# Optimization experiments

Measured on AMD Instinct MI355X. Metric: run time of the kernel, lower is better.

## Reference

```python
import jax, jax.numpy as jnp
import numpy as np

NUM_HEADS = 10
LN_EPS = 1e-5


def setup_inputs() -> dict:
    key = jax.random.key(0)
    ks = jax.random.split(key, 6)
    N, D = 4096, 640  # in_dim == out_dim required by residual add
    x = jax.random.normal(ks[0], (N, D), dtype=jnp.float32)
    s = 1.0 / np.sqrt(D)
    Wq = jax.random.normal(ks[1], (D, D), dtype=jnp.float32) * s  # torch Linear weight [out,in]
    Wk = jax.random.normal(ks[2], (D, D), dtype=jnp.float32) * s
    Wv = jax.random.normal(ks[3], (D, D), dtype=jnp.float32) * s
    gamma = jnp.ones((D,), dtype=jnp.float32)
    beta = jnp.zeros((D,), dtype=jnp.float32)
    return {"x": x, "Wq": Wq, "Wk": Wk, "Wv": Wv, "gamma": gamma, "beta": beta}


def reference(x, Wq, Wk, Wv, gamma, beta):
    N, D = x.shape
    dk = D // NUM_HEADS
    Q = x @ Wq.T  # [N, D]
    K = x @ Wk.T
    V = x @ Wv.T
    # Faithful to source: raw reshapes (NOT transposes)
    Qh = Q.reshape(NUM_HEADS, N, dk)
    Kh = K.reshape(NUM_HEADS, N, dk).reshape(NUM_HEADS, dk, N)  # torch.reshape, not .mT
    Vh = V.reshape(NUM_HEADS, N, dk)
    # Faithful quirk: scale by sqrt(K.shape[2]) == sqrt(N)
    scale = np.float32(np.sqrt(N))
    wghts = jax.nn.softmax((Qh @ Kh) / scale, axis=-1)  # [H, N, N]
    values = wghts @ Vh  # [H, N, dk]
    values = values.reshape(N, NUM_HEADS * dk)  # raw reshape merge
    values = values + x  # residual
    # LayerNorm(out_dim), biased variance, eps=1e-5
    mean = jnp.mean(values, axis=-1, keepdims=True)
    var = jnp.mean(jnp.square(values - mean), axis=-1, keepdims=True)
    out = (values - mean) * jax.lax.rsqrt(var + LN_EPS) * gamma + beta
    return out
```

## Files before the change

### kernel.cpp

```cpp
#include <hip/hip_runtime.h>


typedef __bf16 bf16x8 __attribute__((ext_vector_type(8)));
typedef __bf16 bf16x4 __attribute__((ext_vector_type(4)));
typedef float  f32x4  __attribute__((ext_vector_type(4)));
typedef unsigned short u16x4 __attribute__((ext_vector_type(4)));
typedef short          s16x8 __attribute__((ext_vector_type(8)));

#define N_TOK   4096
#define D_MODEL 640
#define DK      64
#define HSLAB   (N_TOK * DK)
#define EXP2SCL 0.022542110f

#if __has_builtin(__builtin_amdgcn_exp2f)
#define EXP2(x) __builtin_amdgcn_exp2f(x)
#else
#define EXP2(x) exp2f(x)
#endif

__device__ __forceinline__ void stage16(const unsigned short* g, unsigned short* lds_uniform) {
    __builtin_amdgcn_global_load_lds(
        (const __attribute__((address_space(1))) unsigned int*)g,
        (__attribute__((address_space(3))) unsigned int*)lds_uniform, 16, 0, 0);
}

__device__ __forceinline__ u16x4 cvt4(f32x4 v) {
    return __builtin_bit_cast(u16x4, __builtin_convertvector(v, bf16x4));
}

__global__ __launch_bounds__(256) void cvt_all(const float* __restrict__ x,
                                               const float* __restrict__ w0,
                                               const float* __restrict__ w1,
                                               const float* __restrict__ w2,
                                               unsigned short* __restrict__ xb,
                                               unsigned short* __restrict__ d0,
                                               unsigned short* __restrict__ d1,
                                               unsigned short* __restrict__ d2,
                                               f32x4* __restrict__ ltot4) {
    int i = blockIdx.x * 256 + threadIdx.x;
    if (i >= 962560) { ltot4[i - 962560] = (f32x4){0.f, 0.f, 0.f, 0.f}; return; }
    const float* s; unsigned short* d; int off; float scl = 1.0f;
    if (i < 655360) { s = x; d = xb; off = i; }
    else {
        int j = i - 655360;
        int w = j / 102400; off = j - w * 102400;
        s = (w == 0) ? w0 : (w == 1) ? w1 : w2;
        d = (w == 0) ? d0 : (w == 1) ? d1 : d2;
        if (w == 0) scl = EXP2SCL;
    }
    f32x4 v = ((const f32x4*)s)[off];
    v[0] *= scl; v[1] *= scl; v[2] *= scl; v[3] *= scl;
    ((u16x4*)d)[off] = cvt4(v);
}

__global__ __launch_bounds__(256, 2) void gemm_qkv(
    const unsigned short* __restrict__ xb,
    const unsigned short* __restrict__ wq,
    const unsigned short* __restrict__ wk,
    const unsigned short* __restrict__ wv,
    unsigned short* __restrict__ Qo,
    unsigned short* __restrict__ Ko,
    unsigned short* __restrict__ Vo) {
    const int mode = blockIdx.z;
    const unsigned short* W = (mode == 0) ? wq : (mode == 1) ? wk : wv;
    unsigned short*       C = (mode == 0) ? Qo : (mode == 1) ? Ko : Vo;
    const int m0 = blockIdx.y * 128;
    const int n0 = blockIdx.x * 128;

    __shared__ unsigned short As[4096];
    __shared__ unsigned short Bs[4096];

    const int tid  = threadIdx.x;
    const int lane = tid & 63;
    const int wave = tid >> 6;
    const int quad = lane >> 4, l16 = lane & 15;
    const int wm = (wave >> 1) * 64, wn = (wave & 1) * 64;
    const int swz3 = l16 & 3;

    f32x4 acc[4][4] = {};

    const int c0 = wave * 64 + lane, c1 = c0 + 256;
    const int r0 = c0 >> 2, u0 = ((c0 & 3) ^ (r0 & 3)) * 8;
    const int r1 = c1 >> 2, u1 = ((c1 & 3) ^ (r1 & 3)) * 8;
    const int lb0 = (wave * 64) * 8, lb1 = lb0 + 2048;

    for (int kt = 0; kt < D_MODEL; kt += 32) {
        __syncthreads();
        stage16(&xb[(size_t)(m0 + r0) * D_MODEL + kt + u0], As + lb0);
        stage16(&xb[(size_t)(m0 + r1) * D_MODEL + kt + u1], As + lb1);
        stage16(&W [(size_t)(n0 + r0) * D_MODEL + kt + u0], Bs + lb0);
        stage16(&W [(size_t)(n0 + r1) * D_MODEL + kt + u1], Bs + lb1);
        __syncthreads();

        bf16x8 af[4], bfr[4];
        for (int mi = 0; mi < 4; mi++)
            af[mi] = *(const bf16x8*)&As[(wm + mi * 16 + l16) * 32 + (quad ^ swz3) * 8];
        for (int ni = 0; ni < 4; ni++)
            bfr[ni] = *(const bf16x8*)&Bs[(wn + ni * 16 + l16) * 32 + (quad ^ swz3) * 8];
        for (int mi = 0; mi < 4; mi++)
            for (int ni = 0; ni < 4; ni++)
                acc[mi][ni] = __builtin_amdgcn_mfma_f32_16x16x32_bf16(af[mi], bfr[ni], acc[mi][ni], 0, 0, 0);
    }

    for (int mi = 0; mi < 4; mi++)
        for (int ni = 0; ni < 4; ni++) {
            u16x4 cv = cvt4(acc[mi][ni]);
            for (int r = 0; r < 4; r++) {
                int row = m0 + wm + mi * 16 + quad * 4 + r;
                int col = n0 + wn + ni * 16 + l16;
                C[(size_t)row * D_MODEL + col] = cv[r];
            }
        }
}

__global__ __launch_bounds__(256) void transpose_kv(
    const unsigned short* __restrict__ Kn, unsigned short* __restrict__ Kp,
    const unsigned short* __restrict__ Vn, unsigned short* __restrict__ Vp) {
    __shared__ unsigned short T[64][66];
    const int z = blockIdx.z;
    const unsigned short* src; unsigned short* dst;
    int R, Cc, r0, c0;
    if (z < 10) { src = Kn; dst = Kp; R = 64;   Cc = 4096; r0 = 0; c0 = blockIdx.x * 64; }
    else        { src = Vn; dst = Vp; R = 4096; Cc = 64;   r0 = blockIdx.x * 64; c0 = 0; }
    const size_t hb = (size_t)(z % 10) * HSLAB;
    const int t = threadIdx.x;
    const int rr = t >> 3, c8 = (t & 7) * 8;

    for (int hf = 0; hf < 2; hf++) {
        int r = rr + hf * 32;
        bf16x8 v = *(const bf16x8*)&src[hb + (size_t)(r0 + r) * Cc + c0 + c8];
        for (int j = 0; j < 8; j++) T[r][c8 + j] = ((unsigned short*)&v)[j];
    }
    __syncthreads();
    const bf16x8 zz = {};
    for (int hf = 0; hf < 2; hf++) {
        int r = rr + hf * 32;
        *(bf16x8*)&((unsigned short*)src)[hb + (size_t)(r0 + r) * Cc + c0 + c8] = zz;
    }
    for (int hf = 0; hf < 2; hf++) {
        int oc = rr + hf * 32;
        unsigned short v[8];
        for (int j = 0; j < 8; j++) v[j] = T[c8 + j][oc];
        *(bf16x8*)&dst[hb + (size_t)(c0 + oc) * R + r0 + c8] = *(bf16x8*)v;
    }
}

#define PLD 72

__global__ __launch_bounds__(256, 4) void attn(
    const unsigned short* __restrict__ Qb,
    const unsigned short* __restrict__ Kp,
    const unsigned short* __restrict__ Vp,
    float* __restrict__ vals,
    float* __restrict__ l_tot) {
    const int h  = blockIdx.x >> 5;
    const int qt = blockIdx.x & 31;
    const int kbase = blockIdx.y * 1344;
    const int niter = 21 + (blockIdx.y >> 1);
    const int lane = threadIdx.x & 63;
    const int wave = threadIdx.x >> 6;
    const int quad = lane >> 4, l16 = lane & 15;
    const size_t hoff = (size_t)h * HSLAB;

    __shared__ unsigned short Kt[4096];
    __shared__ unsigned short Vt[4096];
    __shared__ unsigned short Pb[4][32 * PLD];
    unsigned short* Pw = &Pb[wave][0];

    const int qbase = qt * 128 + wave * 32;
    bf16x8 qf[2][2];
    for (int g = 0; g < 2; g++)
        for (int kh = 0; kh < 2; kh++)
            qf[g][kh] = *(const bf16x8*)&Qb[hoff + (size_t)(qbase + g * 16 + l16) * DK + kh * 32 + quad * 8];

    f32x4 o[2][4] = {};
    f32x4 ol[2] = {};
    const bf16x8 ones = __builtin_bit_cast(bf16x8, (s16x8)(short)0x3F80);

    const int s0 = wave * 128 + lane;
    const int s1 = s0 + 64;
    const int kr0 = s0 >> 3, kc0 = (s0 & 7) ^ (kr0 & 7);
    const int kr1 = s1 >> 3, kc1 = (s1 & 7) ^ (kr1 & 7);
    const int swz = l16 & 7;

    for (int it = 0; it < niter; it++) {
        const int m0 = kbase + it * 64;
        __syncthreads();
        stage16(Kp + hoff + (size_t)(m0 + kr0) * DK + kc0 * 8, Kt + wave * 1024);
        stage16(Kp + hoff + (size_t)(m0 + kr1) * DK + kc1 * 8, Kt + wave * 1024 + 512);
        stage16(Vp + hoff + (size_t)kr0 * N_TOK + m0 + kc0 * 8, Vt + wave * 1024);
        stage16(Vp + hoff + (size_t)kr1 * N_TOK + m0 + kc1 * 8, Vt + wave * 1024 + 512);
        __syncthreads();

        for (int ni = 0; ni < 4; ni++) {
            const int krow = ni * 16 + l16;
            bf16x8 a0 = *(const bf16x8*)&Kt[krow * 64 + ((0 + quad) ^ swz) * 8];
            bf16x8 a1 = *(const bf16x8*)&Kt[krow * 64 + ((4 + quad) ^ swz) * 8];
            for (int g = 0; g < 2; g++) {
                f32x4 s = {};
                s = __builtin_amdgcn_mfma_f32_16x16x32_bf16(a0, qf[g][0], s, 0, 0, 0);
                s = __builtin_amdgcn_mfma_f32_16x16x32_bf16(a1, qf[g][1], s, 0, 0, 0);
                f32x4 pv;
                for (int r = 0; r < 4; r++) pv[r] = EXP2(s[r]);
                *(u16x4*)&Pw[(g * 16 + l16) * PLD + ni * 16 + quad * 4] = cvt4(pv);
            }
        }

        bf16x8 pf[2][2];
        for (int g = 0; g < 2; g++)
            for (int mh = 0; mh < 2; mh++)
                pf[g][mh] = *(const bf16x8*)&Pw[(g * 16 + l16) * PLD + mh * 32 + quad * 8];

        for (int g = 0; g < 2; g++) {
            ol[g] = __builtin_amdgcn_mfma_f32_16x16x32_bf16(pf[g][0], ones, ol[g], 0, 0, 0);
            ol[g] = __builtin_amdgcn_mfma_f32_16x16x32_bf16(pf[g][1], ones, ol[g], 0, 0, 0);
        }

        for (int nd = 0; nd < 4; nd++) {
            const int vrow = nd * 16 + l16;
            bf16x8 b0 = *(const bf16x8*)&Vt[vrow * 64 + ((0 + quad) ^ swz) * 8];
            bf16x8 b1 = *(const bf16x8*)&Vt[vrow * 64 + ((4 + quad) ^ swz) * 8];
            for (int g = 0; g < 2; g++) {
                o[g][nd] = __builtin_amdgcn_mfma_f32_16x16x32_bf16(pf[g][0], b0, o[g][nd], 0, 0, 0);
                o[g][nd] = __builtin_amdgcn_mfma_f32_16x16x32_bf16(pf[g][1], b1, o[g][nd], 0, 0, 0);
            }
        }
    }

    if (l16 == 0)
        for (int g = 0; g < 2; g++)
            for (int r = 0; r < 4; r++)
                atomicAdd(&l_tot[(h << 12) + qbase + g * 16 + quad * 4 + r], ol[g][r]);

    for (int g = 0; g < 2; g++)
        for (int nd = 0; nd < 4; nd++)
            for (int r = 0; r < 4; r++) {
                int q = qbase + g * 16 + quad * 4 + r;
                atomicAdd(&vals[hoff + (size_t)q * DK + nd * 16 + l16], o[g][nd][r]);
            }
}

__global__ __launch_bounds__(256) void ln_kernel(
    const float* __restrict__ vals, const float* __restrict__ l_tot,
    const float* __restrict__ x,
    const float* __restrict__ gamma, const float* __restrict__ beta,
    float* __restrict__ out) {
    const int wave = threadIdx.x >> 6, lane = threadIdx.x & 63;
    const int row  = blockIdx.x * 4 + wave;
    const float* v  = vals + (size_t)row * D_MODEL;
    const float* xr = x    + (size_t)row * D_MODEL;

    float t[10];
    float s = 0.f;
    for (int i = 0; i < 10; i++) {
        float linv = 1.0f / l_tot[row * 10 + i];
        t[i] = v[lane + i * 64] * linv + xr[lane + i * 64];
        s += t[i];
    }
    for (int off = 32; off; off >>= 1) s += __shfl_xor(s, off, 64);
    float mean = s * (1.0f / 640.0f);
    float s2 = 0.f;
    for (int i = 0; i < 10; i++) { float d = t[i] - mean; s2 += d * d; }
    for (int off = 32; off; off >>= 1) s2 += __shfl_xor(s2, off, 64);
    float inv = rsqrtf(s2 * (1.0f / 640.0f) + 1e-5f);

    float* orow = out + (size_t)row * D_MODEL;
    for (int i = 0; i < 10; i++) {
        int c = lane + i * 64;
        orow[c] = (t[i] - mean) * inv * gamma[c] + beta[c];
    }
}

extern "C" void kernel_launch(void* const* d_in, const int* in_sizes, int n_in,
                              void* d_out, int out_size, void* d_ws, size_t ws_size,
                              hipStream_t stream) {
    const float* x     = (const float*)d_in[0];
    const float* Wq    = (const float*)d_in[1];
    const float* Wk    = (const float*)d_in[2];
    const float* Wv    = (const float*)d_in[3];
    const float* gamma = (const float*)d_in[4];
    const float* beta  = (const float*)d_in[5];
    float* out = (float*)d_out;

    char* ws = (char*)d_ws;
    unsigned short* xb  = (unsigned short*)(ws);
    unsigned short* wqb = (unsigned short*)(ws + 5242880);
    unsigned short* wkb = (unsigned short*)(ws + 6062080);
    unsigned short* wvb = (unsigned short*)(ws + 6881280);
    unsigned short* Qb  = (unsigned short*)(ws + 7700480);
    unsigned short* Kp  = (unsigned short*)(ws + 12943360);
    unsigned short* Vp  = (unsigned short*)(ws + 18186240);
    unsigned short* Kn  = (unsigned short*)(ws + 23429120);
    unsigned short* Vn  = (unsigned short*)(ws + 28672000);
    float*          vals  = (float*)(ws + 23429120);
    float*          l_tot = (float*)(ws + 33914880);

    cvt_all<<<3800, 256, 0, stream>>>(x, Wq, Wk, Wv, xb, wqb, wkb, wvb,
                                      (f32x4*)l_tot);

    gemm_qkv<<<dim3(5, 32, 3), 256, 0, stream>>>(xb, wqb, wkb, wvb, Qb, Kn, Vn);

    transpose_kv<<<dim3(64, 1, 20), 256, 0, stream>>>(Kn, Kp, Vn, Vp);

    attn<<<dim3(320, 3), 256, 0, stream>>>(Qb, Kp, Vp, vals, l_tot);
    ln_kernel<<<1024, 256, 0, stream>>>(vals, l_tot, x, gamma, beta, out);
}
```

Measured before the change: 167.4 us.

## Switch attention to FP8 MFMA with 128-key tiles and FP8 Q/K/V/P

Converts Q, K, V and the softmax probabilities to FP8 e4m3 and runs both attention matmuls with fp8 MFMA instructions. It also enlarges the key tile to 128 and restructures the LDS layout and swizzles for byte elements. The scale is split as a square root across Wq and Wk so Q and K stay within FP8 range. The goals are higher MFMA throughput and half the attention memory traffic, at the cost of lower numeric precision, which may break the accuracy tolerance.

Result: no change. 166.2 us (-0.7%).

```diff
diff --git a/kernel.cpp b/kernel.cpp
--- a/kernel.cpp
+++ b/kernel.cpp
@@ -1,17 +1,20 @@
 #include <hip/hip_runtime.h>
+#if __has_include(<hip/hip_fp8.h>)
+#include <hip/hip_fp8.h>
+#endif
 
 
 typedef __bf16 bf16x8 __attribute__((ext_vector_type(8)));
 typedef __bf16 bf16x4 __attribute__((ext_vector_type(4)));
 typedef float  f32x4  __attribute__((ext_vector_type(4)));
 typedef unsigned short u16x4 __attribute__((ext_vector_type(4)));
-typedef short          s16x8 __attribute__((ext_vector_type(8)));
+typedef unsigned int   u32x4 __attribute__((ext_vector_type(4)));
 
 #define N_TOK   4096
 #define D_MODEL 640
 #define DK      64
 #define HSLAB   (N_TOK * DK)
-#define EXP2SCL 0.022542110f
+#define SQS 0.15014030f
 
 #if __has_builtin(__builtin_amdgcn_exp2f)
 #define EXP2(x) __builtin_amdgcn_exp2f(x)
@@ -19,7 +22,7 @@
 #define EXP2(x) exp2f(x)
 #endif
 
-__device__ __forceinline__ void stage16(const unsigned short* g, unsigned short* lds_uniform) {
+__device__ __forceinline__ void stage16(const void* g, void* lds_uniform) {
     __builtin_amdgcn_global_load_lds(
         (const __attribute__((address_space(1))) unsigned int*)g,
         (__attribute__((address_space(3))) unsigned int*)lds_uniform, 16, 0, 0);
@@ -27,6 +30,22 @@
 
 __device__ __forceinline__ u16x4 cvt4(f32x4 v) {
     return __builtin_bit_cast(u16x4, __builtin_convertvector(v, bf16x4));
+}
+
+__device__ __forceinline__ unsigned int pk_fp8(f32x4 v) {
+#if __has_builtin(__builtin_amdgcn_cvt_pk_fp8_f32)
+    int r = 0;
+    r = __builtin_amdgcn_cvt_pk_fp8_f32(v[0], v[1], r, false);
+    r = __builtin_amdgcn_cvt_pk_fp8_f32(v[2], v[3], r, true);
+    return (unsigned int)r;
+#else
+    union { unsigned char b[4]; unsigned int u; } x;
+    x.b[0] = __hip_fp8_e4m3(v[0]).__x;
+    x.b[1] = __hip_fp8_e4m3(v[1]).__x;
+    x.b[2] = __hip_fp8_e4m3(v[2]).__x;
+    x.b[3] = __hip_fp8_e4m3(v[3]).__x;
+    return x.u;
+#endif
 }
 
 __global__ __launch_bounds__(256) void cvt_all(const float* __restrict__ x,
@@ -47,7 +66,7 @@
         int w = j / 102400; off = j - w * 102400;
         s = (w == 0) ? w0 : (w == 1) ? w1 : w2;
         d = (w == 0) ? d0 : (w == 1) ? d1 : d2;
-        if (w == 0) scl = EXP2SCL;
+        if (w < 2) scl = SQS;
     }
     f32x4 v = ((const f32x4*)s)[off];
     v[0] *= scl; v[1] *= scl; v[2] *= scl; v[3] *= scl;
@@ -115,16 +134,31 @@
 }
 
 __global__ __launch_bounds__(256) void transpose_kv(
-    const unsigned short* __restrict__ Kn, unsigned short* __restrict__ Kp,
-    const unsigned short* __restrict__ Vn, unsigned short* __restrict__ Vp) {
+    const unsigned short* __restrict__ Kn, unsigned char* __restrict__ Kp8,
+    const unsigned short* __restrict__ Vn, unsigned char* __restrict__ Vp8,
+    const unsigned short* __restrict__ Qn, unsigned char* __restrict__ Qf8) {
+    const int z = blockIdx.z;
+    const int t = threadIdx.x;
+
+    if (z >= 20) {
+        const size_t base = (size_t)(z - 20) * HSLAB + blockIdx.x * 4096 + t * 16;
+        bf16x8 v0 = *(const bf16x8*)&Qn[base];
+        bf16x8 v1 = *(const bf16x8*)&Qn[base + 8];
+        f32x4 a = {(float)v0[0], (float)v0[1], (float)v0[2], (float)v0[3]};
+        f32x4 b = {(float)v0[4], (float)v0[5], (float)v0[6], (float)v0[7]};
+        f32x4 c = {(float)v1[0], (float)v1[1], (float)v1[2], (float)v1[3]};
+        f32x4 d = {(float)v1[4], (float)v1[5], (float)v1[6], (float)v1[7]};
+        u32x4 o = {pk_fp8(a), pk_fp8(b), pk_fp8(c), pk_fp8(d)};
+        *(u32x4*)&Qf8[base] = o;
+        return;
+    }
+
     __shared__ unsigned short T[64][66];
-    const int z = blockIdx.z;
-    const unsigned short* src; unsigned short* dst;
+    const unsigned short* src; unsigned char* dst;
     int R, Cc, r0, c0;
-    if (z < 10) { src = Kn; dst = Kp; R = 64;   Cc = 4096; r0 = 0; c0 = blockIdx.x * 64; }
-    else        { src = Vn; dst = Vp; R = 4096; Cc = 64;   r0 = blockIdx.x * 64; c0 = 0; }
+    if (z < 10) { src = Kn; dst = Kp8; R = 64;   Cc = 4096; r0 = 0; c0 = blockIdx.x * 64; }
+    else        { src = Vn; dst = Vp8; R = 4096; Cc = 64;   r0 = blockIdx.x * 64; c0 = 0; }
     const size_t hb = (size_t)(z % 10) * HSLAB;
-    const int t = threadIdx.x;
     const int rr = t >> 3, c8 = (t & 7) * 8;
 
     for (int hf = 0; hf < 2; hf++) {
@@ -140,90 +174,93 @@
     }
     for (int hf = 0; hf < 2; hf++) {
         int oc = rr + hf * 32;
-        unsigned short v[8];
-        for (int j = 0; j < 8; j++) v[j] = T[c8 + j][oc];
-        *(bf16x8*)&dst[hb + (size_t)(c0 + oc) * R + r0 + c8] = *(bf16x8*)v;
-    }
-}
-
-#define PLD 72
+        f32x4 lo, hi;
+        for (int j = 0; j < 4; j++) {
+            lo[j] = __builtin_bit_cast(float, (unsigned int)T[c8 + j][oc] << 16);
+            hi[j] = __builtin_bit_cast(float, (unsigned int)T[c8 + 4 + j][oc] << 16);
+        }
+        uint2 ov; ov.x = pk_fp8(lo); ov.y = pk_fp8(hi);
+        size_t dcol = (z < 10) ? ((size_t)(c0 + oc) * 64 + r0 + c8)
+                               : ((size_t)oc * 4096 + r0 + c8);
+        *(uint2*)&dst[hb + dcol] = ov;
+    }
+}
 
 __global__ __launch_bounds__(256, 4) void attn(
-    const unsigned short* __restrict__ Qb,
-    const unsigned short* __restrict__ Kp,
-    const unsigned short* __restrict__ Vp,
+    const unsigned char* __restrict__ Qf8,
+    const unsigned char* __restrict__ Kp8,
+    const unsigned char* __restrict__ Vp8,
     float* __restrict__ vals,
     float* __restrict__ l_tot) {
     const int h  = blockIdx.x >> 5;
     const int qt = blockIdx.x & 31;
-    const int kbase = blockIdx.y * 1344;
-    const int niter = 21 + (blockIdx.y >> 1);
+    const int ntile = (blockIdx.y == 2) ? 10 : 11;
+    const int tile0 = blockIdx.y * 11;
     const int lane = threadIdx.x & 63;
     const int wave = threadIdx.x >> 6;
     const int quad = lane >> 4, l16 = lane & 15;
     const size_t hoff = (size_t)h * HSLAB;
 
-    __shared__ unsigned short Kt[4096];
-    __shared__ unsigned short Vt[4096];
-    __shared__ unsigned short Pb[4][32 * PLD];
-    unsigned short* Pw = &Pb[wave][0];
+    __shared__ unsigned char sm[32768];
+    unsigned char* Kt = sm;
+    unsigned char* Vt = sm + 8192;
+    unsigned char* Pw = sm + 16384 + wave * 4096;
 
     const int qbase = qt * 128 + wave * 32;
-    bf16x8 qf[2][2];
-    for (int g = 0; g < 2; g++)
-        for (int kh = 0; kh < 2; kh++)
-            qf[g][kh] = *(const bf16x8*)&Qb[hoff + (size_t)(qbase + g * 16 + l16) * DK + kh * 32 + quad * 8];
+    long qd[2][2];
+    for (int g = 0; g < 2; g++) {
+        const unsigned char* qp = Qf8 + hoff + (size_t)(qbase + g * 16 + l16) * 64 + quad * 8;
+        qd[g][0] = *(const long*)(qp);
+        qd[g][1] = *(const long*)(qp + 32);
+    }
 
     f32x4 o[2][4] = {};
     f32x4 ol[2] = {};
-    const bf16x8 ones = __builtin_bit_cast(bf16x8, (s16x8)(short)0x3F80);
-
-    const int s0 = wave * 128 + lane;
-    const int s1 = s0 + 64;
-    const int kr0 = s0 >> 3, kc0 = (s0 & 7) ^ (kr0 & 7);
-    const int kr1 = s1 >> 3, kc1 = (s1 & 7) ^ (kr1 & 7);
-    const int swz = l16 & 7;
-
-    for (int it = 0; it < niter; it++) {
-        const int m0 = kbase + it * 64;
+    const long ONES8 = 0x3838383838383838L;
+
+    const int cA = wave * 64 + lane, cB = cA + 256;
+    const int kA = cA >> 2, uA = ((cA & 3) ^ (kA & 3)) << 4;
+    const int kB = cB >> 2, uB = ((cB & 3) ^ (kB & 3)) << 4;
+    const int dA = cA >> 3, wA = ((cA & 7) ^ (dA & 7)) << 4;
+    const int dB = cB >> 3, wB = ((cB & 7) ^ (dB & 7)) << 4;
+
+    for (int t = 0; t < ntile; t++) {
+        const int keyb = (tile0 + t) << 7;
         __syncthreads();
-        stage16(Kp + hoff + (size_t)(m0 + kr0) * DK + kc0 * 8, Kt + wave * 1024);
-        stage16(Kp + hoff + (size_t)(m0 + kr1) * DK + kc1 * 8, Kt + wave * 1024 + 512);
-        stage16(Vp + hoff + (size_t)kr0 * N_TOK + m0 + kc0 * 8, Vt + wave * 1024);
-        stage16(Vp + hoff + (size_t)kr1 * N_TOK + m0 + kc1 * 8, Vt + wave * 1024 + 512);
+        stage16(Kp8 + hoff + (size_t)(keyb + kA) * 64 + uA, Kt + wave * 1024);
+        stage16(Kp8 + hoff + (size_t)(keyb + kB) * 64 + uB, Kt + 4096 + wave * 1024);
+        stage16(Vp8 + hoff + (size_t)dA * N_TOK + keyb + wA, Vt + wave * 1024);
+        stage16(Vp8 + hoff + (size_t)dB * N_TOK + keyb + wB, Vt + 4096 + wave * 1024);
         __syncthreads();
 
-        for (int ni = 0; ni < 4; ni++) {
-            const int krow = ni * 16 + l16;
-            bf16x8 a0 = *(const bf16x8*)&Kt[krow * 64 + ((0 + quad) ^ swz) * 8];
-            bf16x8 a1 = *(const bf16x8*)&Kt[krow * 64 + ((4 + quad) ^ swz) * 8];
+        for (int ni = 0; ni < 8; ni++) {
+            const int keyloc = ni * 16 + l16;
+            const unsigned char* kp = Kt + keyloc * 64 + (quad & 1) * 8;
+            long a0 = *(const long*)(kp + ((((quad >> 1)    ) ^ (keyloc & 3)) << 4));
+            long a1 = *(const long*)(kp + (((2 + (quad >> 1)) ^ (keyloc & 3)) << 4));
             for (int g = 0; g < 2; g++) {
                 f32x4 s = {};
-                s = __builtin_amdgcn_mfma_f32_16x16x32_bf16(a0, qf[g][0], s, 0, 0, 0);
-                s = __builtin_amdgcn_mfma_f32_16x16x32_bf16(a1, qf[g][1], s, 0, 0, 0);
+                s = __builtin_amdgcn_mfma_f32_16x16x32_fp8_fp8(a0, qd[g][0], s, 0, 0, 0);
+                s = __builtin_amdgcn_mfma_f32_16x16x32_fp8_fp8(a1, qd[g][1], s, 0, 0, 0);
                 f32x4 pv;
                 for (int r = 0; r < 4; r++) pv[r] = EXP2(s[r]);
-                *(u16x4*)&Pw[(g * 16 + l16) * PLD + ni * 16 + quad * 4] = cvt4(pv);
+                *(unsigned int*)(Pw + (g * 16 + l16) * 128 +
+                                 ((ni ^ (l16 & 7)) << 4) + quad * 4) = pk_fp8(pv);
             }
         }
 
-        bf16x8 pf[2][2];
-        for (int g = 0; g < 2; g++)
-            for (int mh = 0; mh < 2; mh++)
-                pf[g][mh] = *(const bf16x8*)&Pw[(g * 16 + l16) * PLD + mh * 32 + quad * 8];
-
-        for (int g = 0; g < 2; g++) {
-            ol[g] = __builtin_amdgcn_mfma_f32_16x16x32_bf16(pf[g][0], ones, ol[g], 0, 0, 0);
-            ol[g] = __builtin_amdgcn_mfma_f32_16x16x32_bf16(pf[g][1], ones, ol[g], 0, 0, 0);
-        }
-
-        for (int nd = 0; nd < 4; nd++) {
-            const int vrow = nd * 16 + l16;
-            bf16x8 b0 = *(const bf16x8*)&Vt[vrow * 64 + ((0 + quad) ^ swz) * 8];
-            bf16x8 b1 = *(const bf16x8*)&Vt[vrow * 64 + ((4 + quad) ^ swz) * 8];
+        for (int ks = 0; ks < 4; ks++) {
+            const int ub = (ks << 1) + (quad >> 1);
+            long vf[4];
+            for (int nd = 0; nd < 4; nd++) {
+                const int dkl = nd * 16 + l16;
+                vf[nd] = *(const long*)(Vt + dkl * 128 + ((ub ^ (dkl & 7)) << 4) + (quad & 1) * 8);
+            }
             for (int g = 0; g < 2; g++) {
-                o[g][nd] = __builtin_amdgcn_mfma_f32_16x16x32_bf16(pf[g][0], b0, o[g][nd], 0, 0, 0);
-                o[g][nd] = __builtin_amdgcn_mfma_f32_16x16x32_bf16(pf[g][1], b1, o[g][nd], 0, 0, 0);
+                long pf = *(const long*)(Pw + (g * 16 + l16) * 128 + ((ub ^ (l16 & 7)) << 4) + (quad & 1) * 8);
+                ol[g] = __builtin_amdgcn_mfma_f32_16x16x32_fp8_fp8(pf, ONES8, ol[g], 0, 0, 0);
+                for (int nd = 0; nd < 4; nd++)
+                    o[g][nd] = __builtin_amdgcn_mfma_f32_16x16x32_fp8_fp8(pf, vf[nd], o[g][nd], 0, 0, 0);
             }
         }
     }
@@ -285,12 +322,13 @@
 
     char* ws = (char*)d_ws;
     unsigned short* xb  = (unsigned short*)(ws);
+    unsigned char*  Qf8 = (unsigned char*)(ws);
     unsigned short* wqb = (unsigned short*)(ws + 5242880);
     unsigned short* wkb = (unsigned short*)(ws + 6062080);
     unsigned short* wvb = (unsigned short*)(ws + 6881280);
-    unsigned short* Qb  = (unsigned short*)(ws + 7700480);
-    unsigned short* Kp  = (unsigned short*)(ws + 12943360);
-    unsigned short* Vp  = (unsigned short*)(ws + 18186240);
+    unsigned short* Qn  = (unsigned short*)(ws + 7700480);
+    unsigned char*  Kp8 = (unsigned char*)(ws + 12943360);
+    unsigned char*  Vp8 = (unsigned char*)(ws + 18186240);
     unsigned short* Kn  = (unsigned short*)(ws + 23429120);
     unsigned short* Vn  = (unsigned short*)(ws + 28672000);
     float*          vals  = (float*)(ws + 23429120);
@@ -299,10 +337,10 @@
     cvt_all<<<3800, 256, 0, stream>>>(x, Wq, Wk, Wv, xb, wqb, wkb, wvb,
                                       (f32x4*)l_tot);
 
-    gemm_qkv<<<dim3(5, 32, 3), 256, 0, stream>>>(xb, wqb, wkb, wvb, Qb, Kn, Vn);
-
-    transpose_kv<<<dim3(64, 1, 20), 256, 0, stream>>>(Kn, Kp, Vn, Vp);
-
-    attn<<<dim3(320, 3), 256, 0, stream>>>(Qb, Kp, Vp, vals, l_tot);
+    gemm_qkv<<<dim3(5, 32, 3), 256, 0, stream>>>(xb, wqb, wkb, wvb, Qn, Kn, Vn);
+
+    transpose_kv<<<dim3(64, 1, 30), 256, 0, stream>>>(Kn, Kp8, Vn, Vp8, Qn, Qf8);
+
+    attn<<<dim3(320, 3), 256, 0, stream>>>(Qf8, Kp8, Vp8, vals, l_tot);
     ln_kernel<<<1024, 256, 0, stream>>>(vals, l_tot, x, gamma, beta, out);
 }
```
